# Optimization experiments

Hardware: AMD Instinct MI355X
Metric: run time of the kernel (lower is better)

## Reference

```python
import jax, jax.numpy as jnp
import numpy as np

N = 50000
E = 800000
H = 128
K_CONVS = 3
K_HOPS = 3


def setup_inputs() -> dict:
    key = jax.random.key(0)
    ks = jax.random.split(key, 8)
    x = jax.random.normal(ks[0], (N, H), dtype=jnp.float32)
    edge_index = jax.random.randint(ks[1], (2, E), 0, N, dtype=jnp.int64)
    s = 1.0 / np.sqrt(H)
    # MPlayer edge MLP: Linear(2H->H), LeakyReLU(0.2), Linear(H->H)
    W1 = jax.random.normal(ks[2], (2 * H, H), dtype=jnp.float32) * (1.0 / np.sqrt(2 * H))
    b1 = jnp.zeros((H,), jnp.float32)
    W2 = jax.random.normal(ks[3], (H, H), dtype=jnp.float32) * s
    b2 = jnp.zeros((H,), jnp.float32)
    # TAGConv stack: K_CONVS layers, each with K_HOPS+1 weight mats [H,H] + bias
    tag_w = jax.random.normal(ks[4], (K_CONVS, K_HOPS + 1, H, H), dtype=jnp.float32) * s
    tag_b = jnp.zeros((K_CONVS, H), jnp.float32)
    return {"x": x, "edge_index": edge_index, "W1": W1, "b1": b1,
            "W2": W2, "b2": b2, "tag_w": tag_w, "tag_b": tag_b}


def _mp_layer(x, src, dst, W1, b1, W2, b2):
    # gather -> concat -> 2-layer MLP per edge -> scatter-add at dst
    h = jnp.concatenate([x[dst], x[src]], axis=-1)  # [E, 2H] (x_i=dst, x_j=src)
    h = jax.nn.leaky_relu(h @ W1 + b1, negative_slope=0.2)
    m = h @ W2 + b2
    return jax.ops.segment_sum(m, dst, num_segments=N)


def _tag_conv(x, src, dst, norm, Ws, b):
    # out = sum_k A_norm^k x @ W_k + b  (PyG TAGConv, add_self_loops=False)
    out = x @ Ws[0]
    for k in range(1, Ws.shape[0]):
        x = jax.ops.segment_sum(norm[:, None] * x[src], dst, num_segments=N)
        out = out + x @ Ws[k]
    return out + b


def reference(x, edge_index, W1, b1, W2, b2, tag_w, tag_b):
    src = edge_index[0]
    dst = edge_index[1]
    # symmetric gcn_norm without self-loops (degree counted at target=dst)
    deg = jax.ops.segment_sum(jnp.ones((E,), x.dtype), dst, num_segments=N)
    dinv = jnp.where(deg > 0, jax.lax.rsqrt(jnp.maximum(deg, 1e-12)), 0.0)
    norm = dinv[src] * dinv[dst]  # [E]

    x = _mp_layer(x, src, dst, W1, b1, W2, b2)
    for i in range(K_CONVS):
        x = _tag_conv(x, src, dst, norm, tag_w[i], tag_b[i])
        x = jax.nn.relu(x)
    return x
```

## Files before the change

kernel.cpp:

```cpp
#include <hip/hip_runtime.h>

#define NN 50000
#define NE 800000
#define HH 128
#define SCAN_BLK 256
#define NBLK ((NN + SCAN_BLK - 1) / SCAN_BLK)

typedef _Float16 half8 __attribute__((ext_vector_type(8)));
typedef _Float16 half4 __attribute__((ext_vector_type(4)));
typedef _Float16 half2t __attribute__((ext_vector_type(2)));
typedef float floatx16 __attribute__((ext_vector_type(16)));

static inline size_t align256(size_t x) { return (x + 255) & ~(size_t)255; }

__global__ void k_deg(const int* __restrict__ dst, int* __restrict__ deg) {
    int e = blockIdx.x * 256 + threadIdx.x;
    if (e < NE) atomicAdd(&deg[dst[e]], 1);
}

__global__ void k_bsum(const int* __restrict__ deg, int* __restrict__ part) {
    __shared__ int sd[SCAN_BLK];
    int t = threadIdx.x;
    int i = blockIdx.x * SCAN_BLK + t;
    sd[t] = (i < NN) ? deg[i] : 0;
    __syncthreads();
    for (int off = SCAN_BLK / 2; off > 0; off >>= 1) {
        if (t < off) sd[t] += sd[t + off];
        __syncthreads();
    }
    if (t == 0) part[blockIdx.x] = sd[0];
}

__global__ void k_scanpart(const int* __restrict__ part, int* __restrict__ partoff) {
    __shared__ int sd[SCAN_BLK];
    int t = threadIdx.x;
    int v = (t < NBLK) ? part[t] : 0;
    sd[t] = v;
    __syncthreads();
    for (int off = 1; off < SCAN_BLK; off <<= 1) {
        int add = (t >= off) ? sd[t - off] : 0;
        __syncthreads();
        sd[t] += add;
        __syncthreads();
    }
    if (t < NBLK) partoff[t] = sd[t] - v;
}

__global__ void k_apply(const int* __restrict__ deg, const int* __restrict__ partoff,
                        int* __restrict__ offsets, float* __restrict__ dinv) {
    __shared__ int sd[SCAN_BLK];
    int t = threadIdx.x;
    int i = blockIdx.x * SCAN_BLK + t;
    int v = (i < NN) ? deg[i] : 0;
    sd[t] = v;
    __syncthreads();
    for (int off = 1; off < SCAN_BLK; off <<= 1) {
        int add = (t >= off) ? sd[t - off] : 0;
        __syncthreads();
        sd[t] += add;
        __syncthreads();
    }
    if (i < NN) {
        offsets[i] = partoff[blockIdx.x] + sd[t] - v;
        dinv[i] = (v > 0) ? rsqrtf((float)v) : 0.0f;
    }
    if (i == 0) offsets[NN] = NE;
}

__global__ void k_fill(const int* __restrict__ src, const int* __restrict__ dst,
                       const int* __restrict__ offsets, int* __restrict__ cursor,
                       const float* __restrict__ dinv,
                       int* __restrict__ csrc, float* __restrict__ cnorm) {
    int e = blockIdx.x * 256 + threadIdx.x;
    if (e >= NE) return;
    int s = src[e], d = dst[e];
    int pos = atomicAdd(&cursor[d], 1);
    int idx = offsets[d] + pos;
    csrc[idx] = s;
    cnorm[idx] = dinv[s] * dinv[d];
}

__global__ void k_cvt_x(const float* __restrict__ x, _Float16* __restrict__ xh) {
    int i = blockIdx.x * 256 + threadIdx.x;
    if (i * 4 < NN * HH) {
        float4 v = *(const float4*)(x + (size_t)i * 4);
        half4 h;
        h.x = (_Float16)v.x; h.y = (_Float16)v.y;
        h.z = (_Float16)v.z; h.w = (_Float16)v.w;
        *(half4*)(xh + (size_t)i * 4) = h;
    }
}

__global__ void k_cvt_w(const float* __restrict__ W1, const float* __restrict__ W2,
                        const float* __restrict__ tw,
                        _Float16* __restrict__ W1tP, _Float16* __restrict__ W1tQ,
                        _Float16* __restrict__ W2t, _Float16* __restrict__ TWt) {
    int i = blockIdx.x * 256 + threadIdx.x;
    if (i < 16384) {
        int c = i >> 7, k = i & 127;
        W1tP[c * 128 + k] = (_Float16)W1[k * 128 + c];
        W1tQ[c * 128 + k] = (_Float16)W1[(128 + k) * 128 + c];
    } else if (i < 32768) {
        int j = i - 16384;
        int c = j >> 7, k = j & 127;
        W2t[c * 128 + k] = (_Float16)W2[k * 128 + c];
    } else if (i < 32768 + 3 * 65536) {
        int j = i - 32768;
        int L = j >> 16;
        int c = (j >> 9) & 127;
        int k = j & 511;
        TWt[(size_t)L * 65536 + c * 512 + k] =
            (_Float16)tw[(size_t)L * 65536 + (size_t)(k >> 7) * 16384 + (size_t)(k & 127) * 128 + c];
    }
}

template <int KDIM, int HAS_BIAS, int HAS_DEG, int RELU, typename OutT>
__global__ __launch_bounds__(256) void k_mm(
    const _Float16* __restrict__ A, int lda,
    const _Float16* __restrict__ Bt,
    const float* __restrict__ bias, const int* __restrict__ deg,
    OutT* __restrict__ Out, int ldo, int nrows) {
    __shared__ _Float16 As[128 * 64];
    __shared__ _Float16 Bs[128 * 64];
    const int t = threadIdx.x;
    const int l = t & 63;
    const int w = t >> 6;
    const int wm = w >> 1, wn = w & 1;
    const int row0 = blockIdx.x * 128;

    floatx16 acc[2][2] = {};

    const int srow = t >> 3;
    const int sslot = t & 7;

    for (int c = 0; c < KDIM / 64; ++c) {
        __syncthreads();
#pragma unroll
        for (int p = 0; p < 4; ++p) {
            int r = srow + p * 32;
            int g = row0 + r;
            uint4 v = make_uint4(0, 0, 0, 0);
            if (g < nrows) v = *(const uint4*)(A + (size_t)g * lda + c * 64 + sslot * 8);
            *(uint4*)((char*)As + r * 128 + ((sslot * 16) ^ ((r & 7) << 4))) = v;
        }
#pragma unroll
        for (int p = 0; p < 4; ++p) {
            int r = srow + p * 32;
            uint4 v = *(const uint4*)(Bt + (size_t)r * KDIM + c * 64 + sslot * 8);
            *(uint4*)((char*)Bs + r * 128 + ((sslot * 16) ^ ((r & 7) << 4))) = v;
        }
        __syncthreads();
#pragma unroll
        for (int ks = 0; ks < 4; ++ks) {
            const int koff = ks * 32 + (l >> 5) * 16;
            half8 a0, a1, b0, b1;
            { int r = wm * 64 + (l & 31);      a0 = *(const half8*)((const char*)As + r * 128 + (koff ^ ((r & 7) << 4))); }
            { int r = wm * 64 + 32 + (l & 31); a1 = *(const half8*)((const char*)As + r * 128 + (koff ^ ((r & 7) << 4))); }
            { int r = wn * 64 + (l & 31);      b0 = *(const half8*)((const char*)Bs + r * 128 + (koff ^ ((r & 7) << 4))); }
            { int r = wn * 64 + 32 + (l & 31); b1 = *(const half8*)((const char*)Bs + r * 128 + (koff ^ ((r & 7) << 4))); }
            acc[0][0] = __builtin_amdgcn_mfma_f32_32x32x16_f16(a0, b0, acc[0][0], 0, 0, 0);
            acc[0][1] = __builtin_amdgcn_mfma_f32_32x32x16_f16(a0, b1, acc[0][1], 0, 0, 0);
            acc[1][0] = __builtin_amdgcn_mfma_f32_32x32x16_f16(a1, b0, acc[1][0], 0, 0, 0);
            acc[1][1] = __builtin_amdgcn_mfma_f32_32x32x16_f16(a1, b1, acc[1][1], 0, 0, 0);
        }
    }

#pragma unroll
    for (int mf = 0; mf < 2; ++mf) {
#pragma unroll
        for (int nf = 0; nf < 2; ++nf) {
            const int col = wn * 64 + nf * 32 + (l & 31);
            const float bc = HAS_BIAS ? bias[col] : 0.0f;
#pragma unroll
            for (int r = 0; r < 16; ++r) {
                int row = wm * 64 + mf * 32 + 4 * (l >> 5) + (r & 3) + 8 * (r >> 2);
                int g = row0 + row;
                if (g < nrows) {
                    float v = acc[mf][nf][r];
                    if (HAS_BIAS) v += (HAS_DEG ? (float)deg[g] : 1.0f) * bc;
                    if (RELU) v = fmaxf(v, 0.0f);
                    Out[(size_t)g * ldo + col] = (OutT)v;
                }
            }
        }
    }
}

__global__ void k_edge_mp(_Float16* __restrict__ PQ, const int* __restrict__ offsets,
                          const int* __restrict__ csrc) {
    const int n = blockIdx.x;
    const int j = threadIdx.x;
    const int beg = offsets[n], end = offsets[n + 1];
    half2t p2 = *(const half2t*)(PQ + (size_t)n * 256 + 2 * j);
    const float p0 = (float)p2.x, p1 = (float)p2.y;
    float a0 = 0.f, a1 = 0.f;
    int i = beg;
    for (; i + 2 <= end; i += 2) {
        int s0 = csrc[i], s1 = csrc[i + 1];
        half2t q0 = *(const half2t*)(PQ + (size_t)s0 * 256 + 128 + 2 * j);
        half2t q1 = *(const half2t*)(PQ + (size_t)s1 * 256 + 128 + 2 * j);
        float v00 = p0 + (float)q0.x, v01 = p1 + (float)q0.y;
        float v10 = p0 + (float)q1.x, v11 = p1 + (float)q1.y;
        a0 += ((v00 > 0.f) ? v00 : 0.2f * v00) + ((v10 > 0.f) ? v10 : 0.2f * v10);
        a1 += ((v01 > 0.f) ? v01 : 0.2f * v01) + ((v11 > 0.f) ? v11 : 0.2f * v11);
    }
    if (i < end) {
        int s = csrc[i];
        half2t q = *(const half2t*)(PQ + (size_t)s * 256 + 128 + 2 * j);
        float v0 = p0 + (float)q.x, v1 = p1 + (float)q.y;
        a0 += (v0 > 0.f) ? v0 : 0.2f * v0;
        a1 += (v1 > 0.f) ? v1 : 0.2f * v1;
    }
    half2t o; o.x = (_Float16)a0; o.y = (_Float16)a1;
    *(half2t*)(PQ + (size_t)n * 256 + 2 * j) = o;
}

__global__ void k_spmm(const _Float16* __restrict__ Xin, _Float16* __restrict__ Yout,
                       const int* __restrict__ offsets, const int* __restrict__ csrc,
                       const float* __restrict__ cnorm) {
    const int n = blockIdx.x;
    const int j = threadIdx.x;
    const int beg = offsets[n], end = offsets[n + 1];
    float a0 = 0.f, a1 = 0.f;
    int i = beg;
    for (; i + 2 <= end; i += 2) {
        int s0 = csrc[i], s1 = csrc[i + 1];
        float n0 = cnorm[i], n1 = cnorm[i + 1];
        half2t v0 = *(const half2t*)(Xin + (size_t)s0 * 512 + 2 * j);
        half2t v1 = *(const half2t*)(Xin + (size_t)s1 * 512 + 2 * j);
        a0 += n0 * (float)v0.x + n1 * (float)v1.x;
        a1 += n0 * (float)v0.y + n1 * (float)v1.y;
    }
    if (i < end) {
        int s = csrc[i];
        float nv = cnorm[i];
        half2t v = *(const half2t*)(Xin + (size_t)s * 512 + 2 * j);
        a0 += nv * (float)v.x;
        a1 += nv * (float)v.y;
    }
    half2t o; o.x = (_Float16)a0; o.y = (_Float16)a1;
    *(half2t*)(Yout + (size_t)n * 512 + 2 * j) = o;
}

extern "C" void kernel_launch(void* const* d_in, const int* in_sizes, int n_in,
                              void* d_out, int out_size, void* d_ws, size_t ws_size,
                              hipStream_t stream) {
    const float* x  = (const float*)d_in[0];
    const int*   ei = (const int*)d_in[1];
    const float* W1 = (const float*)d_in[2];
    const float* b1 = (const float*)d_in[3];
    const float* W2 = (const float*)d_in[4];
    const float* b2 = (const float*)d_in[5];
    const float* tw = (const float*)d_in[6];
    const float* tb = (const float*)d_in[7];
    float* out = (float*)d_out;

    const int* srcp = ei;
    const int* dstp = ei + NE;

    char* p = (char*)d_ws;
    auto alloc = [&](size_t bytes) { char* r = p; p += align256(bytes); return r; };
    int*       deg     = (int*)alloc((size_t)NN * 4);
    int*       cursor  = (int*)alloc((size_t)NN * 4);
    int*       offsets = (int*)alloc((size_t)(NN + 1) * 4);
    float*     dinv    = (float*)alloc((size_t)NN * 4);
    int*       part    = (int*)alloc((size_t)NBLK * 4);
    int*       partoff = (int*)alloc((size_t)NBLK * 4);
    int*       csrc    = (int*)alloc((size_t)NE * 4);
    float*     cnorm   = (float*)alloc((size_t)NE * 4);
    _Float16*  xh      = (_Float16*)alloc((size_t)NN * HH * 2);
    _Float16*  PQ      = (_Float16*)alloc((size_t)NN * 256 * 2);
    _Float16*  X4      = (_Float16*)alloc((size_t)NN * 512 * 2);
    _Float16*  W1tP    = (_Float16*)alloc(16384 * 2);
    _Float16*  W1tQ    = (_Float16*)alloc(16384 * 2);
    _Float16*  W2t     = (_Float16*)alloc(16384 * 2);
    _Float16*  TWt     = (_Float16*)alloc((size_t)3 * 65536 * 2);

    hipMemsetAsync(deg, 0, (size_t)NN * 4, stream);
    hipMemsetAsync(cursor, 0, (size_t)NN * 4, stream);

    k_deg<<<(NE + 255) / 256, 256, 0, stream>>>(dstp, deg);
    k_bsum<<<NBLK, SCAN_BLK, 0, stream>>>(deg, part);
    k_scanpart<<<1, SCAN_BLK, 0, stream>>>(part, partoff);
    k_apply<<<NBLK, SCAN_BLK, 0, stream>>>(deg, partoff, offsets, dinv);
    k_fill<<<(NE + 255) / 256, 256, 0, stream>>>(srcp, dstp, offsets, cursor, dinv, csrc, cnorm);

    k_cvt_x<<<(NN * HH / 4 + 255) / 256, 256, 0, stream>>>(x, xh);
    k_cvt_w<<<(32768 + 3 * 65536 + 255) / 256, 256, 0, stream>>>(W1, W2, tw, W1tP, W1tQ, W2t, TWt);

    const int mmgrid = (NN + 127) / 128;

    k_mm<128, 1, 0, 0, _Float16><<<mmgrid, 256, 0, stream>>>(xh, HH, W1tP, b1, nullptr, PQ, 256, NN);
    k_mm<128, 0, 0, 0, _Float16><<<mmgrid, 256, 0, stream>>>(xh, HH, W1tQ, nullptr, nullptr, PQ + 128, 256, NN);
    k_edge_mp<<<NN, 64, 0, stream>>>(PQ, offsets, csrc);
    k_mm<128, 1, 1, 0, _Float16><<<mmgrid, 256, 0, stream>>>(PQ, 256, W2t, b2, deg, X4, 512, NN);

    for (int L = 0; L < 3; ++L) {
        const _Float16* Wt = TWt + (size_t)L * 65536;
        const float* bL = tb + (size_t)L * 128;
        k_spmm<<<NN, 64, 0, stream>>>(X4 + 0,   X4 + 128, offsets, csrc, cnorm);
        k_spmm<<<NN, 64, 0, stream>>>(X4 + 128, X4 + 256, offsets, csrc, cnorm);
        k_spmm<<<NN, 64, 0, stream>>>(X4 + 256, X4 + 384, offsets, csrc, cnorm);
        if (L < 2) {
            k_mm<512, 1, 0, 1, _Float16><<<mmgrid, 256, 0, stream>>>(X4, 512, Wt, bL, nullptr, X4, 512, NN);
        } else {
            k_mm<512, 1, 0, 1, float><<<mmgrid, 256, 0, stream>>>(X4, 512, Wt, bL, nullptr, out, HH, NN);
        }
    }
}
```

Before: 575.6 us.

## Pack CSR edges and process 8 nodes per block with half4 lanes

Source index and normalization are interleaved into one uint2 edge array, so each edge needs a single 8-byte load instead of two separate loads. The edge message-passing and SpMM kernels now map 32 lanes to one node, each lane handling 4 halves, and pack 8 nodes into a 256-thread block instead of using one 64-thread block per node. The inner loops are unrolled by 4 to keep more gathers in flight. This cuts block-scheduling overhead and widens memory accesses, at the cost of 32-lane groups that do not fill a 64-wide wavefront evenly when neighbouring nodes have different degrees.

```diff
diff --git a/kernel.cpp b/kernel.cpp
--- a/kernel.cpp
+++ b/kernel.cpp
@@ -5,10 +5,10 @@
 #define HH 128
 #define SCAN_BLK 256
 #define NBLK ((NN + SCAN_BLK - 1) / SCAN_BLK)
+#define NB8 ((NN + 7) / 8)
 
 typedef _Float16 half8 __attribute__((ext_vector_type(8)));
 typedef _Float16 half4 __attribute__((ext_vector_type(4)));
-typedef _Float16 half2t __attribute__((ext_vector_type(2)));
 typedef float floatx16 __attribute__((ext_vector_type(16)));
 
 static inline size_t align256(size_t x) { return (x + 255) & ~(size_t)255; }
@@ -69,15 +69,14 @@
 
 __global__ void k_fill(const int* __restrict__ src, const int* __restrict__ dst,
                        const int* __restrict__ offsets, int* __restrict__ cursor,
-                       const float* __restrict__ dinv,
-                       int* __restrict__ csrc, float* __restrict__ cnorm) {
+                       const float* __restrict__ dinv, uint2* __restrict__ epk) {
     int e = blockIdx.x * 256 + threadIdx.x;
     if (e >= NE) return;
     int s = src[e], d = dst[e];
     int pos = atomicAdd(&cursor[d], 1);
     int idx = offsets[d] + pos;
-    csrc[idx] = s;
-    cnorm[idx] = dinv[s] * dinv[d];
+    float nv = dinv[s] * dinv[d];
+    epk[idx] = make_uint2((unsigned)s, __float_as_uint(nv));
 }
 
 __global__ void k_cvt_x(const float* __restrict__ x, _Float16* __restrict__ xh) {
@@ -186,60 +185,79 @@
     }
 }
 
-__global__ void k_edge_mp(_Float16* __restrict__ PQ, const int* __restrict__ offsets,
-                          const int* __restrict__ csrc) {
-    const int n = blockIdx.x;
-    const int j = threadIdx.x;
+__global__ __launch_bounds__(256) void k_edge_mp(_Float16* __restrict__ PQ,
+                                                 const int* __restrict__ offsets,
+                                                 const uint2* __restrict__ epk) {
+    const int t = threadIdx.x;
+    const int n = blockIdx.x * 8 + (t >> 5);
+    if (n >= NN) return;
+    const int lane = t & 31;
     const int beg = offsets[n], end = offsets[n + 1];
-    half2t p2 = *(const half2t*)(PQ + (size_t)n * 256 + 2 * j);
-    const float p0 = (float)p2.x, p1 = (float)p2.y;
-    float a0 = 0.f, a1 = 0.f;
+    half4 p4 = *(const half4*)(PQ + (size_t)n * 256 + lane * 4);
+    const float p0 = (float)p4.x, p1 = (float)p4.y, p2 = (float)p4.z, p3 = (float)p4.w;
+    float a0 = 0.f, a1 = 0.f, a2 = 0.f, a3 = 0.f;
     int i = beg;
-    for (; i + 2 <= end; i += 2) {
-        int s0 = csrc[i], s1 = csrc[i + 1];
-        half2t q0 = *(const half2t*)(PQ + (size_t)s0 * 256 + 128 + 2 * j);
-        half2t q1 = *(const half2t*)(PQ + (size_t)s1 * 256 + 128 + 2 * j);
-        float v00 = p0 + (float)q0.x, v01 = p1 + (float)q0.y;
-        float v10 = p0 + (float)q1.x, v11 = p1 + (float)q1.y;
-        a0 += ((v00 > 0.f) ? v00 : 0.2f * v00) + ((v10 > 0.f) ? v10 : 0.2f * v10);
-        a1 += ((v01 > 0.f) ? v01 : 0.2f * v01) + ((v11 > 0.f) ? v11 : 0.2f * v11);
-    }
-    if (i < end) {
-        int s = csrc[i];
-        half2t q = *(const half2t*)(PQ + (size_t)s * 256 + 128 + 2 * j);
-        float v0 = p0 + (float)q.x, v1 = p1 + (float)q.y;
-        a0 += (v0 > 0.f) ? v0 : 0.2f * v0;
-        a1 += (v1 > 0.f) ? v1 : 0.2f * v1;
-    }
-    half2t o; o.x = (_Float16)a0; o.y = (_Float16)a1;
-    *(half2t*)(PQ + (size_t)n * 256 + 2 * j) = o;
-}
-
-__global__ void k_spmm(const _Float16* __restrict__ Xin, _Float16* __restrict__ Yout,
-                       const int* __restrict__ offsets, const int* __restrict__ csrc,
-                       const float* __restrict__ cnorm) {
-    const int n = blockIdx.x;
-    const int j = threadIdx.x;
+#define LRELU4(vx, vy, vz, vw)                                        \
+    a0 += ((vx) > 0.f) ? (vx) : 0.2f * (vx);                          \
+    a1 += ((vy) > 0.f) ? (vy) : 0.2f * (vy);                          \
+    a2 += ((vz) > 0.f) ? (vz) : 0.2f * (vz);                          \
+    a3 += ((vw) > 0.f) ? (vw) : 0.2f * (vw);
+    for (; i + 4 <= end; i += 4) {
+        uint2 e0 = epk[i + 0], e1 = epk[i + 1], e2 = epk[i + 2], e3 = epk[i + 3];
+        half4 q0 = *(const half4*)(PQ + (size_t)e0.x * 256 + 128 + lane * 4);
+        half4 q1 = *(const half4*)(PQ + (size_t)e1.x * 256 + 128 + lane * 4);
+        half4 q2 = *(const half4*)(PQ + (size_t)e2.x * 256 + 128 + lane * 4);
+        half4 q3 = *(const half4*)(PQ + (size_t)e3.x * 256 + 128 + lane * 4);
+        LRELU4(p0 + (float)q0.x, p1 + (float)q0.y, p2 + (float)q0.z, p3 + (float)q0.w)
+        LRELU4(p0 + (float)q1.x, p1 + (float)q1.y, p2 + (float)q1.z, p3 + (float)q1.w)
+        LRELU4(p0 + (float)q2.x, p1 + (float)q2.y, p2 + (float)q2.z, p3 + (float)q2.w)
+        LRELU4(p0 + (float)q3.x, p1 + (float)q3.y, p2 + (float)q3.z, p3 + (float)q3.w)
+    }
+    for (; i < end; ++i) {
+        uint2 e = epk[i];
+        half4 q = *(const half4*)(PQ + (size_t)e.x * 256 + 128 + lane * 4);
+        LRELU4(p0 + (float)q.x, p1 + (float)q.y, p2 + (float)q.z, p3 + (float)q.w)
+    }
+#undef LRELU4
+    half4 o;
+    o.x = (_Float16)a0; o.y = (_Float16)a1; o.z = (_Float16)a2; o.w = (_Float16)a3;
+    *(half4*)(PQ + (size_t)n * 256 + lane * 4) = o;
+}
+
+__global__ __launch_bounds__(256) void k_spmm(const _Float16* __restrict__ Xin,
+                                              _Float16* __restrict__ Yout,
+                                              const int* __restrict__ offsets,
+                                              const uint2* __restrict__ epk) {
+    const int t = threadIdx.x;
+    const int n = blockIdx.x * 8 + (t >> 5);
+    if (n >= NN) return;
+    const int lane = t & 31;
     const int beg = offsets[n], end = offsets[n + 1];
-    float a0 = 0.f, a1 = 0.f;
+    float a0 = 0.f, a1 = 0.f, a2 = 0.f, a3 = 0.f;
     int i = beg;
-    for (; i + 2 <= end; i += 2) {
-        int s0 = csrc[i], s1 = csrc[i + 1];
-        float n0 = cnorm[i], n1 = cnorm[i + 1];
-        half2t v0 = *(const half2t*)(Xin + (size_t)s0 * 512 + 2 * j);
-        half2t v1 = *(const half2t*)(Xin + (size_t)s1 * 512 + 2 * j);
-        a0 += n0 * (float)v0.x + n1 * (float)v1.x;
-        a1 += n0 * (float)v0.y + n1 * (float)v1.y;
-    }
-    if (i < end) {
-        int s = csrc[i];
-        float nv = cnorm[i];
-        half2t v = *(const half2t*)(Xin + (size_t)s * 512 + 2 * j);
-        a0 += nv * (float)v.x;
-        a1 += nv * (float)v.y;
-    }
-    half2t o; o.x = (_Float16)a0; o.y = (_Float16)a1;
-    *(half2t*)(Yout + (size_t)n * 512 + 2 * j) = o;
+    for (; i + 4 <= end; i += 4) {
+        uint2 e0 = epk[i + 0], e1 = epk[i + 1], e2 = epk[i + 2], e3 = epk[i + 3];
+        half4 v0 = *(const half4*)(Xin + (size_t)e0.x * 512 + lane * 4);
+        half4 v1 = *(const half4*)(Xin + (size_t)e1.x * 512 + lane * 4);
+        half4 v2 = *(const half4*)(Xin + (size_t)e2.x * 512 + lane * 4);
+        half4 v3 = *(const half4*)(Xin + (size_t)e3.x * 512 + lane * 4);
+        float n0 = __uint_as_float(e0.y), n1 = __uint_as_float(e1.y);
+        float n2 = __uint_as_float(e2.y), n3 = __uint_as_float(e3.y);
+        a0 += n0 * (float)v0.x + n1 * (float)v1.x + n2 * (float)v2.x + n3 * (float)v3.x;
+        a1 += n0 * (float)v0.y + n1 * (float)v1.y + n2 * (float)v2.y + n3 * (float)v3.y;
+        a2 += n0 * (float)v0.z + n1 * (float)v1.z + n2 * (float)v2.z + n3 * (float)v3.z;
+        a3 += n0 * (float)v0.w + n1 * (float)v1.w + n2 * (float)v2.w + n3 * (float)v3.w;
+    }
+    for (; i < end; ++i) {
+        uint2 e = epk[i];
+        float nv = __uint_as_float(e.y);
+        half4 v = *(const half4*)(Xin + (size_t)e.x * 512 + lane * 4);
+        a0 += nv * (float)v.x; a1 += nv * (float)v.y;
+        a2 += nv * (float)v.z; a3 += nv * (float)v.w;
+    }
+    half4 o;
+    o.x = (_Float16)a0; o.y = (_Float16)a1; o.z = (_Float16)a2; o.w = (_Float16)a3;
+    *(half4*)(Yout + (size_t)n * 512 + lane * 4) = o;
 }
 
 extern "C" void kernel_launch(void* const* d_in, const int* in_sizes, int n_in,
@@ -266,8 +284,7 @@
     float*     dinv    = (float*)alloc((size_t)NN * 4);
     int*       part    = (int*)alloc((size_t)NBLK * 4);
     int*       partoff = (int*)alloc((size_t)NBLK * 4);
-    int*       csrc    = (int*)alloc((size_t)NE * 4);
-    float*     cnorm   = (float*)alloc((size_t)NE * 4);
+    uint2*     epk     = (uint2*)alloc((size_t)NE * 8);
     _Float16*  xh      = (_Float16*)alloc((size_t)NN * HH * 2);
     _Float16*  PQ      = (_Float16*)alloc((size_t)NN * 256 * 2);
     _Float16*  X4      = (_Float16*)alloc((size_t)NN * 512 * 2);
@@ -283,7 +300,7 @@
     k_bsum<<<NBLK, SCAN_BLK, 0, stream>>>(deg, part);
     k_scanpart<<<1, SCAN_BLK, 0, stream>>>(part, partoff);
     k_apply<<<NBLK, SCAN_BLK, 0, stream>>>(deg, partoff, offsets, dinv);
-    k_fill<<<(NE + 255) / 256, 256, 0, stream>>>(srcp, dstp, offsets, cursor, dinv, csrc, cnorm);
+    k_fill<<<(NE + 255) / 256, 256, 0, stream>>>(srcp, dstp, offsets, cursor, dinv, epk);
 
     k_cvt_x<<<(NN * HH / 4 + 255) / 256, 256, 0, stream>>>(x, xh);
     k_cvt_w<<<(32768 + 3 * 65536 + 255) / 256, 256, 0, stream>>>(W1, W2, tw, W1tP, W1tQ, W2t, TWt);
@@ -292,15 +309,15 @@
 
     k_mm<128, 1, 0, 0, _Float16><<<mmgrid, 256, 0, stream>>>(xh, HH, W1tP, b1, nullptr, PQ, 256, NN);
     k_mm<128, 0, 0, 0, _Float16><<<mmgrid, 256, 0, stream>>>(xh, HH, W1tQ, nullptr, nullptr, PQ + 128, 256, NN);
-    k_edge_mp<<<NN, 64, 0, stream>>>(PQ, offsets, csrc);
+    k_edge_mp<<<NB8, 256, 0, stream>>>(PQ, offsets, epk);
     k_mm<128, 1, 1, 0, _Float16><<<mmgrid, 256, 0, stream>>>(PQ, 256, W2t, b2, deg, X4, 512, NN);
 
     for (int L = 0; L < 3; ++L) {
         const _Float16* Wt = TWt + (size_t)L * 65536;
         const float* bL = tb + (size_t)L * 128;
-        k_spmm<<<NN, 64, 0, stream>>>(X4 + 0,   X4 + 128, offsets, csrc, cnorm);
-        k_spmm<<<NN, 64, 0, stream>>>(X4 + 128, X4 + 256, offsets, csrc, cnorm);
-        k_spmm<<<NN, 64, 0, stream>>>(X4 + 256, X4 + 384, offsets, csrc, cnorm);
+        k_spmm<<<NB8, 256, 0, stream>>>(X4 + 0,   X4 + 128, offsets, epk);
+        k_spmm<<<NB8, 256, 0, stream>>>(X4 + 128, X4 + 256, offsets, epk);
+        k_spmm<<<NB8, 256, 0, stream>>>(X4 + 256, X4 + 384, offsets, epk);
         if (L < 2) {
             k_mm<512, 1, 0, 1, _Float16><<<mmgrid, 256, 0, stream>>>(X4, 512, Wt, bL, nullptr, X4, 512, NN);
         } else {
```

After: 529.4 us. 8.0% less time.
